# Kernel tuning notes

Hardware: AMD Instinct MI355X
Metric: run time of the kernel (lower is better)

Reference implementation:

```python
import jax, jax.numpy as jnp
import numpy as np

I_DIM, L_DIM, H_DIM, O_DIM = 1024, 1024, 2048, 512
HALT_H = max(4, H_DIM // 2)
BATCH = 4096


def setup_inputs() -> dict:
    key = jax.random.key(0)
    ks = jax.random.split(key, 14)
    s = 0.02
    gin = I_DIM + O_DIM
    jdim = L_DIM + O_DIM
    return {
        "inputs": jax.random.normal(ks[0], (BATCH, I_DIM), jnp.float32),
        "W_ih": jax.random.normal(ks[1], (3 * L_DIM, gin), jnp.float32) * s,
        "W_hh": jax.random.normal(ks[2], (3 * L_DIM, L_DIM), jnp.float32) * s,
        "b_ih": jax.random.normal(ks[3], (3 * L_DIM,), jnp.float32) * s,
        "b_hh": jax.random.normal(ks[4], (3 * L_DIM,), jnp.float32) * s,
        "aw1": jax.random.normal(ks[5], (H_DIM, jdim), jnp.float32) * s,
        "ab1": jax.random.normal(ks[6], (H_DIM,), jnp.float32) * s,
        "aw2": jax.random.normal(ks[7], (O_DIM, H_DIM), jnp.float32) * s,
        "ab2": jax.random.normal(ks[8], (O_DIM,), jnp.float32) * s,
        "hw1": jax.random.normal(ks[9], (HALT_H, jdim), jnp.float32) * s,
        "hb1": jax.random.normal(ks[10], (HALT_H,), jnp.float32) * s,
        "hw2": jax.random.normal(ks[11], (2, HALT_H), jnp.float32) * s,
        "hb2": jax.random.normal(ks[12], (2,), jnp.float32) * s,
        "inner_cycles": 4,
        "outer_steps": 8,
    }


def reference(inputs, W_ih, W_hh, b_ih, b_hh, aw1, ab1, aw2, ab2,
              hw1, hb1, hw2, hb2, inner_cycles, outer_steps):
    B = inputs.shape[0]
    L = W_hh.shape[1]
    O = aw2.shape[0]

    def gru_step(state, x_gates):
        # PyTorch GRUCell: gates ordered (r, z, n)
        h_gates = state @ W_hh.T + b_hh  # [B, 3L]
        xr, xz, xn = jnp.split(x_gates, 3, axis=-1)
        hr, hz, hn = jnp.split(h_gates, 3, axis=-1)
        r = jax.nn.sigmoid(xr + hr)
        z = jax.nn.sigmoid(xz + hz)
        n = jnp.tanh(xn + r * hn)
        return (1.0 - z) * n + z * state

    def outer(carry, _):
        state, ans = carry
        # gru_input is constant over inner cycles -> hoist input projection
        x = jnp.concatenate([inputs, ans], axis=-1)       # [B, I+O]
        x_gates = x @ W_ih.T + b_ih                        # [B, 3L]

        def inner(s, _):
            return gru_step(s, x_gates), None

        state, _ = jax.lax.scan(inner, state, None, length=inner_cycles)
        joint = jnp.concatenate([state, ans], axis=-1)     # [B, L+O]
        h1 = jax.nn.relu(joint @ aw1.T + ab1)
        logits = h1 @ aw2.T + ab2                          # [B, O]
        ans_new = jnp.tanh(logits)
        h2 = jax.nn.relu(joint @ hw1.T + hb1)
        halt = h2 @ hw2.T + hb2                            # [B, 2]
        return (state, ans_new), (logits, halt)

    state0 = jnp.zeros((B, L), inputs.dtype)
    ans0 = jnp.zeros((B, O), inputs.dtype)
    _, (answer_logits, halt_logits) = jax.lax.scan(
        outer, (state0, ans0), None, length=outer_steps)
    # stacked equivalents of the per-step lists: [outer_steps, B, O], [outer_steps, B, 2]
    return answer_logits, halt_logits
```

## Files before the change

### kernel.cpp

```cpp
#include <hip/hip_runtime.h>
#include <math.h>

#define BATCH 4096
#define LDIM 1024
#define HDIM 2048
#define ODIM 512
#define GDIM 3072
#define JDIM 1536
#define INNER 4
#define OUTER 8

using f16 = _Float16;
using f16x4 = __attribute__((ext_vector_type(4))) _Float16;
using f16x8 = __attribute__((ext_vector_type(8))) _Float16;
using f32x4 = __attribute__((ext_vector_type(4))) float;

typedef __attribute__((address_space(3))) void lds_void;
typedef __attribute__((address_space(1))) void glob_void;

__device__ __forceinline__ void gload16(const void* g, void* l) {
  __builtin_amdgcn_global_load_lds((const glob_void*)g, (lds_void*)l, 16, 0, 0);
}

#define MFMA16(a, b, c) __builtin_amdgcn_mfma_f32_16x16x32_f16(a, b, c, 0, 0, 0)
#define WAIT_VM(N) asm volatile("s_waitcnt vmcnt(" #N ")" ::: "memory")
#define SBAR asm volatile("s_barrier" ::: "memory")

__device__ __forceinline__ float fast_sigmoid(float x) {
  return __builtin_amdgcn_rcpf(1.0f + __expf(-x));
}
__device__ __forceinline__ float fast_tanh(float x) {
  return 1.0f - 2.0f * __builtin_amdgcn_rcpf(1.0f + __expf(2.0f * x));
}

__global__ __launch_bounds__(256) void convert_w(const float* __restrict__ src,
                                                 f16* __restrict__ dst, int n4) {
  int i = blockIdx.x * 256 + threadIdx.x;
  if (i >= n4) return;
  float4 v = ((const float4*)src)[i];
  f16x4 d = {(f16)v.x, (f16)v.y, (f16)v.z, (f16)v.w};
  *(f16x4*)&dst[(size_t)i * 4] = d;
}

__global__ __launch_bounds__(256) void convert_w2(const float* __restrict__ src,
                                                  f16* __restrict__ dst) {
  int idx = blockIdx.x * 256 + threadIdx.x;
  if (idx >= GDIM * 128) return;
  int row = idx >> 7, c4 = idx & 127;
  float4 v = *(const float4*)&src[(size_t)row * JDIM + 1024 + c4 * 4];
  f16x4 d = {(f16)v.x, (f16)v.y, (f16)v.z, (f16)v.w};
  *(f16x4*)&dst[(size_t)row * 512 + c4 * 4] = d;
}

template <int EPI>
__global__ __launch_bounds__(512, 1) void gemm_f16(
    const f16* __restrict__ A, const f16* __restrict__ W,
    const float* __restrict__ bias, const float* __restrict__ bias2,
    const f16* __restrict__ Xb,
    f16* __restrict__ Ch, f16* __restrict__ Cf, int N, int K, int lda, int ldw) {
  __shared__ f16 sA[2 * 2 * 128 * 32];
  __shared__ f16 sW[2 * 2 * 384 * 32];
  const int tid = threadIdx.x;
  const int w = tid >> 6, lane = tid & 63;
  const int wm = w >> 2, wn = w & 3;
  const int fr = lane & 15, quad = lane >> 4;
  const int nb = N / 384;
  const int m0 = (blockIdx.x / nb) * 128, n0 = (blockIdx.x % nb) * 384;

  const int swz_src = (((tid & 3) ^ ((tid >> 3) & 3)) * 8);
  const f16* pAst = A + (size_t)(m0 + (tid >> 2)) * lda + swz_src;
  const f16* pWst = W + (size_t)(n0 + (tid >> 2)) * ldw + swz_src;
  const size_t h128w = (size_t)128 * ldw;
  const int swr = ((quad ^ ((fr >> 1) & 3)) * 8);

  f32x4 acc[4][6] = {};
  const int NT = K >> 6;

#define STA(p, kh, kt)                                                \
  {                                                                   \
    int o = ((p) * 2 + (kh)) * 4096 + tid * 8;                        \
    gload16(pAst + (kt) * 64 + (kh) * 32, &sA[o]);                    \
  }
#define STW(p, kh, kt)                                                \
  {                                                                   \
    int o = ((p) * 2 + (kh)) * 12288 + tid * 8;                       \
    gload16(pWst + (kt) * 64 + (kh) * 32, &sW[o]);                    \
    gload16(pWst + h128w + (kt) * 64 + (kh) * 32, &sW[o + 4096]);     \
    gload16(pWst + 2 * h128w + (kt) * 64 + (kh) * 32, &sW[o + 8192]); \
  }
#define LDA(p, kk)                                                    \
  _Pragma("unroll") for (int i2 = 0; i2 < 4; ++i2) {                  \
    int rm = wm * 64 + i2 * 16 + fr;                                  \
    af[i2] = *(const f16x8*)&sA[((p) * 2 + (kk)) * 4096 + rm * 32 + swr]; \
  }
#define LDB(p, kk, nh)                                                \
  _Pragma("unroll") for (int j2 = 0; j2 < 3; ++j2) {                  \
    int rn = wn * 96 + ((nh) * 3 + j2) * 16 + fr;                     \
    bf[j2] = *(const f16x8*)&sW[((p) * 2 + (kk)) * 12288 + rn * 32 + swr]; \
  }
#define DOMFMA(nh)                                                    \
  __builtin_amdgcn_s_setprio(1);                                      \
  _Pragma("unroll") for (int i2 = 0; i2 < 4; ++i2)                    \
  _Pragma("unroll") for (int j2 = 0; j2 < 3; ++j2)                    \
      acc[i2][(nh) * 3 + j2] = MFMA16(af[i2], bf[j2], acc[i2][(nh) * 3 + j2]); \
  __builtin_amdgcn_s_setprio(0);

  STA(0, 0, 0); STW(0, 0, 0); STA(0, 1, 0); STW(0, 1, 0);

  for (int t = 0; t < NT; ++t) {
    const int p = t & 1, pn = p ^ 1;
    const bool pf = (t + 1 < NT);
    f16x8 af[4], bf[3];
    if (t == NT - 1) { WAIT_VM(0); } else { WAIT_VM(4); }
    SBAR;
    if (pf) STA(pn, 0, t + 1);
    LDA(p, 0); LDB(p, 0, 0);
    DOMFMA(0);
    SBAR;
    if (pf) STW(pn, 0, t + 1);
    LDB(p, 0, 1);
    DOMFMA(1);
    if (t == NT - 1) { WAIT_VM(0); } else { WAIT_VM(4); }
    SBAR;
    if (pf) STA(pn, 1, t + 1);
    LDA(p, 1); LDB(p, 1, 0);
    DOMFMA(0);
    SBAR;
    if (pf) STW(pn, 1, t + 1);
    LDB(p, 1, 1);
    DOMFMA(1);
  }
#undef STA
#undef STW
#undef LDA
#undef LDB
#undef DOMFMA

#pragma unroll
  for (int j = 0; j < 6; ++j) {
    int n = n0 + wn * 96 + j * 16 + fr;
    float bv;
    if (EPI == 3) bv = 0.0f;
    else if (EPI == 1) bv = (n < 2048) ? bias[n] : bias2[n - 2048];
    else bv = bias[n];
#pragma unroll
    for (int i = 0; i < 4; ++i) {
      int mb = m0 + wm * 64 + i * 16 + quad * 4;
      if (EPI == 0) {
        f16x4 o = {(f16)(acc[i][j][0] + bv), (f16)(acc[i][j][1] + bv),
                   (f16)(acc[i][j][2] + bv), (f16)(acc[i][j][3] + bv)};
        *(f16x4*)&Ch[((size_t)(mb >> 2) * N + n) * 4] = o;
      } else if (EPI == 3) {
        size_t off = ((size_t)(mb >> 2) * N + n) * 4;
        f16x4 b4 = *(const f16x4*)&Xb[off];
        f16x4 o = {(f16)(acc[i][j][0] + (float)b4[0]),
                   (f16)(acc[i][j][1] + (float)b4[1]),
                   (f16)(acc[i][j][2] + (float)b4[2]),
                   (f16)(acc[i][j][3] + (float)b4[3])};
        *(f16x4*)&Ch[off] = o;
      } else {
#pragma unroll
        for (int r = 0; r < 4; ++r) {
          int m = mb + r;
          float v = fmaxf(acc[i][j][r] + bv, 0.0f);
          if (n < 2048)
            Ch[(size_t)m * HDIM + n] = (f16)v;
          else
            Cf[(size_t)m * LDIM + (n - 2048)] = (f16)v;
        }
      }
    }
  }
}

__global__ __launch_bounds__(256, 2) void gemm_logits(
    const f16* __restrict__ A, const f16* __restrict__ W,
    const float* __restrict__ bias, float* __restrict__ Cout,
    f16* __restrict__ aJH, int N, int K) {
  __shared__ f16 sA[3][128 * 32];
  __shared__ f16 sW[3][64 * 32];
  const int tid = threadIdx.x;
  const int w = tid >> 6, lane = tid & 63;
  const int fr = lane & 15, quad = lane >> 4;
  const int m0 = blockIdx.y * 128, n0 = blockIdx.x * 64;
  const int swz_src = (((tid & 3) ^ ((tid >> 3) & 3)) * 8);
  const f16* pA = A + (size_t)(m0 + (tid >> 2)) * K + swz_src;
  const f16* pW = W + (size_t)(n0 + (tid >> 2)) * K + swz_src;
  const size_t rstep = (size_t)64 * K;
  const int swr = ((quad ^ ((fr >> 1) & 3)) * 8);

  f32x4 acc[2][4] = {};
  const int NT = K >> 5;

  auto stage = [&](int b, int k) {
    gload16(pA + k, &sA[b][tid * 8]);
    gload16(pA + rstep + k, &sA[b][tid * 8 + 2048]);
    gload16(pW + k, &sW[b][tid * 8]);
  };
  stage(0, 0);
  stage(1, 32);
  int bb = 0;
  for (int t = 0; t < NT; ++t) {
    if (t == NT - 1) { WAIT_VM(0); } else { WAIT_VM(3); }
    __builtin_amdgcn_s_barrier();
    if (t + 2 < NT) {
      int bn = bb + 2; if (bn >= 3) bn -= 3;
      stage(bn, (t + 2) * 32);
    }
    f16x8 af[2], bf[4];
#pragma unroll
    for (int i = 0; i < 2; ++i) {
      int rm = w * 32 + i * 16 + fr;
      af[i] = *(const f16x8*)&sA[bb][rm * 32 + swr];
    }
#pragma unroll
    for (int j = 0; j < 4; ++j) {
      int rn = j * 16 + fr;
      bf[j] = *(const f16x8*)&sW[bb][rn * 32 + swr];
    }
    __builtin_amdgcn_s_setprio(1);
#pragma unroll
    for (int i = 0; i < 2; ++i)
#pragma unroll
      for (int j = 0; j < 4; ++j) acc[i][j] = MFMA16(af[i], bf[j], acc[i][j]);
    __builtin_amdgcn_s_setprio(0);
    if (++bb == 3) bb = 0;
  }

#pragma unroll
  for (int j = 0; j < 4; ++j) {
    int n = n0 + j * 16 + fr;
    float bv = bias[n];
#pragma unroll
    for (int i = 0; i < 2; ++i) {
      int mb = m0 + w * 32 + i * 16 + quad * 4;
#pragma unroll
      for (int r = 0; r < 4; ++r) {
        int m = mb + r;
        float v = acc[i][j][r] + bv;
        Cout[(size_t)m * N + n] = v;
        aJH[(size_t)m * JDIM + 1024 + n] = (f16)fast_tanh(v);
      }
    }
  }
}

__global__ __launch_bounds__(256, 2) void gru_fused(
    const f16* __restrict__ inJ, const f16* __restrict__ Whh,
    const float* __restrict__ bhh, const f16* __restrict__ xgP,
    f16* __restrict__ outJ) {
  __shared__ f16 sA[3][128 * 32];
  __shared__ f16 sW0[3][64 * 32];
  __shared__ f16 sW1[3][64 * 32];
  __shared__ f16 sW2[3][64 * 32];
  const int tid = threadIdx.x;
  const int w = tid >> 6, lane = tid & 63;
  const int fr = lane & 15, quad = lane >> 4;
  const int flat = blockIdx.x;
  const int xcd = flat & 7, local = flat >> 3;
  const int n0 = (xcd * 2 + (local & 1)) * 64;
  const int m0 = (local >> 1) * 128;
  const int srow = w * 32 + (lane >> 2);
  const int scol = (((lane & 3) ^ ((lane >> 3) & 3)) * 8);
  const f16* pA = inJ + (size_t)(m0 + srow) * JDIM + scol;
  const size_t rstepA = (size_t)16 * JDIM;
  const int wrow = w * 16 + (lane >> 2);
  const f16* pW0 = Whh + (size_t)(n0 + wrow) * LDIM + scol;
  const f16* pW1 = pW0 + (size_t)LDIM * LDIM;
  const f16* pW2 = pW1 + (size_t)LDIM * LDIM;
  const int loA = w * 1024, loW = w * 512;

  f32x4 ar[2][4] = {}, az[2][4] = {}, an_[2][4] = {};
  const int NT = LDIM >> 5;

  auto stage = [&](int b, int k) {
    gload16(pA + k, &sA[b][loA]);
    gload16(pA + rstepA + k, &sA[b][loA + 512]);
    gload16(pW0 + k, &sW0[b][loW]);
    gload16(pW1 + k, &sW1[b][loW]);
    gload16(pW2 + k, &sW2[b][loW]);
  };
  stage(0, 0);
  stage(1, 32);
  int bb = 0;
  for (int t = 0; t < NT; ++t) {
    if (t == NT - 1) { WAIT_VM(0); } else { WAIT_VM(5); }
    __builtin_amdgcn_s_barrier();
    if (t + 2 < NT) {
      int bn = bb + 2; if (bn >= 3) bn -= 3;
      stage(bn, (t + 2) * 32);
    }
    f16x8 a_[2], w0[4], w1[4], w2[4];
#pragma unroll
    for (int i = 0; i < 2; ++i) {
      int rr = w * 32 + i * 16 + fr;
      a_[i] = *(const f16x8*)&sA[bb][rr * 32 + ((quad ^ ((rr >> 1) & 3)) << 3)];
    }
#pragma unroll
    for (int j = 0; j < 4; ++j) {
      int rw = j * 16 + fr;
      int wo = rw * 32 + ((quad ^ ((rw >> 1) & 3)) << 3);
      w0[j] = *(const f16x8*)&sW0[bb][wo];
      w1[j] = *(const f16x8*)&sW1[bb][wo];
      w2[j] = *(const f16x8*)&sW2[bb][wo];
    }
    __builtin_amdgcn_s_setprio(1);
#pragma unroll
    for (int i = 0; i < 2; ++i)
#pragma unroll
      for (int j = 0; j < 4; ++j) {
        ar[i][j] = MFMA16(a_[i], w0[j], ar[i][j]);
        az[i][j] = MFMA16(a_[i], w1[j], az[i][j]);
        an_[i][j] = MFMA16(a_[i], w2[j], an_[i][j]);
      }
    __builtin_amdgcn_s_setprio(0);
    if (++bb == 3) bb = 0;
  }

#pragma unroll
  for (int j = 0; j < 4; ++j) {
    int col = n0 + j * 16 + fr;
    float br = bhh[col], bz = bhh[col + LDIM], bn = bhh[col + 2 * LDIM];
#pragma unroll
    for (int i = 0; i < 2; ++i) {
      int mb = m0 + w * 32 + i * 16 + quad * 4;
      size_t xb = ((size_t)(mb >> 2) * GDIM + col) * 4;
      f16x4 x4r = *(const f16x4*)&xgP[xb];
      f16x4 x4z = *(const f16x4*)&xgP[xb + (size_t)LDIM * 4];
      f16x4 x4n = *(const f16x4*)&xgP[xb + (size_t)2 * LDIM * 4];
#pragma unroll
      for (int r = 0; r < 4; ++r) {
        int m = mb + r;
        size_t si = (size_t)m * JDIM + col;
        float sold = (float)inJ[si];
        float rg = fast_sigmoid((float)x4r[r] + ar[i][j][r] + br);
        float zg = fast_sigmoid((float)x4z[r] + az[i][j][r] + bz);
        float ng = fast_tanh((float)x4n[r] + rg * (an_[i][j][r] + bn));
        float o = (1.0f - zg) * ng + zg * sold;
        outJ[si] = (f16)o;
      }
    }
  }
}

__global__ __launch_bounds__(256) void halt_kernel(
    const f16* __restrict__ h2, const float* __restrict__ hw2,
    const float* __restrict__ hb2, float* __restrict__ out) {
  int wave = (blockIdx.x * 256 + threadIdx.x) >> 6;
  int lane = threadIdx.x & 63;
  if (wave >= BATCH) return;
  const f16* row = h2 + (size_t)wave * LDIM;
  float s0 = 0.0f, s1 = 0.0f;
#pragma unroll
  for (int k = lane; k < LDIM; k += 64) {
    float v = (float)row[k];
    s0 = fmaf(v, hw2[k], s0);
    s1 = fmaf(v, hw2[LDIM + k], s1);
  }
#pragma unroll
  for (int off = 32; off > 0; off >>= 1) {
    s0 += __shfl_xor(s0, off);
    s1 += __shfl_xor(s1, off);
  }
  if (lane == 0) {
    out[(size_t)wave * 2 + 0] = s0 + hb2[0];
    out[(size_t)wave * 2 + 1] = s1 + hb2[1];
  }
}

extern "C" void kernel_launch(void* const* d_in, const int* in_sizes, int n_in,
                              void* d_out, int out_size, void* d_ws, size_t ws_size,
                              hipStream_t stream) {
  const float* inputs = (const float*)d_in[0];
  const float* W_ih = (const float*)d_in[1];
  const float* W_hh = (const float*)d_in[2];
  const float* b_ih = (const float*)d_in[3];
  const float* b_hh = (const float*)d_in[4];
  const float* aw1 = (const float*)d_in[5];
  const float* ab1 = (const float*)d_in[6];
  const float* aw2 = (const float*)d_in[7];
  const float* ab2 = (const float*)d_in[8];
  const float* hw1 = (const float*)d_in[9];
  const float* hb1 = (const float*)d_in[10];
  const float* hw2 = (const float*)d_in[11];
  const float* hb2 = (const float*)d_in[12];

  float* out = (float*)d_out;
  float* logits_out = out;
  float* halt_out = out + (size_t)OUTER * BATCH * ODIM;

  char* p = (char*)d_ws;
  auto take = [&](size_t bytes) { char* q = p; p += (bytes + 255) & ~255ull; return q; };
  f16* xg = (f16*)take((size_t)BATCH * GDIM * 2);
  f16* inpF16 = xg;
  f16* WihF = xg + (size_t)BATCH * LDIM;
  f16* xgBase = (f16*)take((size_t)BATCH * GDIM * 2);
  f16* J0 = (f16*)take((size_t)BATCH * JDIM * 2);
  f16* J1 = (f16*)take((size_t)BATCH * JDIM * 2);
  f16* h2F = (f16*)take((size_t)BATCH * LDIM * 2);
  f16* WhhF = (f16*)take((size_t)GDIM * LDIM * 2);
  f16* WjF = (f16*)take((size_t)(HDIM + LDIM) * JDIM * 2);
  f16* aw2F = (f16*)take((size_t)ODIM * HDIM * 2);
  f16* W2F = (f16*)take((size_t)GDIM * 512 * 2);
  f16* h1 = xg;
  if ((size_t)(p - (char*)d_ws) > ws_size) return;

  (void)hipMemsetAsync(J0, 0, (size_t)BATCH * JDIM * 2, stream);

  auto conv = [&](const float* s, f16* d, size_t n) {
    int n4 = (int)(n / 4);
    convert_w<<<(n4 + 255) / 256, 256, 0, stream>>>(s, d, n4);
  };
  conv(inputs, inpF16, (size_t)BATCH * LDIM);
  conv(W_ih, WihF, (size_t)GDIM * JDIM);
  convert_w2<<<(GDIM * 128 + 255) / 256, 256, 0, stream>>>(W_ih, W2F);
  conv(W_hh, WhhF, (size_t)GDIM * LDIM);
  conv(aw1, WjF, (size_t)HDIM * JDIM);
  conv(hw1, WjF + (size_t)HDIM * JDIM, (size_t)LDIM * JDIM);
  conv(aw2, aw2F, (size_t)ODIM * HDIM);

  gemm_f16<0><<<(BATCH / 128) * (GDIM / 384), 512, 0, stream>>>(
      inpF16, WihF, b_ih, nullptr, nullptr, xgBase, nullptr,
      GDIM, LDIM, LDIM, JDIM);

  for (int s = 0; s < OUTER; ++s) {
    const f16* xgUse = xgBase;
    if (s > 0) {
      gemm_f16<3><<<(BATCH / 128) * (GDIM / 384), 512, 0, stream>>>(
          J0 + 1024, W2F, nullptr, nullptr, xgBase, xg, nullptr,
          GDIM, 512, JDIM, 512);
      xgUse = xg;
    }
    gru_fused<<<512, 256, 0, stream>>>(J0, WhhF, b_hh, xgUse, J1);
    gru_fused<<<512, 256, 0, stream>>>(J1, WhhF, b_hh, xgUse, J0);
    gru_fused<<<512, 256, 0, stream>>>(J0, WhhF, b_hh, xgUse, J1);
    gru_fused<<<512, 256, 0, stream>>>(J1, WhhF, b_hh, xgUse, J0);
    gemm_f16<1><<<(BATCH / 128) * ((HDIM + LDIM) / 384), 512, 0, stream>>>(
        J0, WjF, ab1, hb1, nullptr, h1, h2F, HDIM + LDIM, JDIM, JDIM, JDIM);
    gemm_logits<<<dim3(ODIM / 64, BATCH / 128), 256, 0, stream>>>(
        h1, aw2F, ab2, logits_out + (size_t)s * BATCH * ODIM, J0, ODIM, HDIM);
    halt_kernel<<<BATCH / 4, 256, 0, stream>>>(
        h2F, hw2, hb2, halt_out + (size_t)s * BATCH * 2);
  }
}
```

Baseline: 2.371 ms.

## Enlarge GRU and joint-MLP GEMM tiles for more operand reuse

The GRU kernel now uses 512-thread blocks, each computing a 128x128 tile per gate across 256 blocks instead of 128x64 tiles across 512 blocks. This changes the warp layout to 2x4 and drops the XCD-aware block mapping. A new 256x256-tile GEMM kernel replaces the 128x384 one for the joint MLP layer, with a per-block epilogue choosing between the h1 and h2 outputs. Both changes aim to cut global/LDS traffic per FLOP, at the cost of fewer blocks (lower occupancy, worse tail balance) and more registers per thread.

Result: slower. 2.523 ms (+6.4%).

```diff
diff --git a/kernel.cpp b/kernel.cpp
--- a/kernel.cpp
+++ b/kernel.cpp
@@ -53,11 +53,125 @@
 }
 
 template <int EPI>
-__global__ __launch_bounds__(512, 1) void gemm_f16(
+__global__ __launch_bounds__(512, 1) void gemm_256(
     const f16* __restrict__ A, const f16* __restrict__ W,
     const float* __restrict__ bias, const float* __restrict__ bias2,
     const f16* __restrict__ Xb,
     f16* __restrict__ Ch, f16* __restrict__ Cf, int N, int K, int lda, int ldw) {
+  __shared__ f16 sA[2 * 2 * 256 * 32];
+  __shared__ f16 sW[2 * 2 * 256 * 32];
+  const int tid = threadIdx.x;
+  const int w = tid >> 6, lane = tid & 63;
+  const int wm = w >> 2, wn = w & 3;
+  const int fr = lane & 15, quad = lane >> 4;
+  const int nb = N >> 8;
+  const int m0 = (blockIdx.x / nb) * 256, n0 = (blockIdx.x % nb) * 256;
+
+  const int swz_src = (((tid & 3) ^ ((tid >> 3) & 3)) * 8);
+  const f16* pAst = A + (size_t)(m0 + (tid >> 2)) * lda + swz_src;
+  const f16* pWst = W + (size_t)(n0 + (tid >> 2)) * ldw + swz_src;
+  const size_t h128a = (size_t)128 * lda;
+  const size_t h128w = (size_t)128 * ldw;
+  const int ldst = tid * 8;
+  const int swr = ((quad ^ ((fr >> 1) & 3)) * 8);
+
+  f32x4 acc[8][4] = {};
+  const int NT = K >> 6;
+
+#define STA(p, kh, kt)                                              \
+  {                                                                 \
+    int o = ((p) * 2 + (kh)) * 8192 + ldst;                         \
+    gload16(pAst + (kt) * 64 + (kh) * 32, &sA[o]);                  \
+    gload16(pAst + h128a + (kt) * 64 + (kh) * 32, &sA[o + 4096]);   \
+  }
+#define STW(p, kh, kt)                                              \
+  {                                                                 \
+    int o = ((p) * 2 + (kh)) * 8192 + ldst;                         \
+    gload16(pWst + (kt) * 64 + (kh) * 32, &sW[o]);                  \
+    gload16(pWst + h128w + (kt) * 64 + (kh) * 32, &sW[o + 4096]);   \
+  }
+#define LDB(p, kk)                                                  \
+  _Pragma("unroll") for (int j = 0; j < 4; ++j) {                   \
+    int rn = wn * 64 + j * 16 + fr;                                 \
+    bf[j] = *(const f16x8*)&sW[((p) * 2 + (kk)) * 8192 + rn * 32 + swr]; \
+  }
+#define LDA(p, kk, mh)                                              \
+  _Pragma("unroll") for (int i2 = 0; i2 < 4; ++i2) {                \
+    int rm = wm * 128 + (mh) * 64 + i2 * 16 + fr;                   \
+    af[i2] = *(const f16x8*)&sA[((p) * 2 + (kk)) * 8192 + rm * 32 + swr]; \
+  }
+#define DOMFMA(mh)                                                  \
+  __builtin_amdgcn_s_setprio(1);                                    \
+  _Pragma("unroll") for (int i2 = 0; i2 < 4; ++i2)                  \
+  _Pragma("unroll") for (int j = 0; j < 4; ++j)                     \
+      acc[(mh) * 4 + i2][j] = MFMA16(af[i2], bf[j], acc[(mh) * 4 + i2][j]); \
+  __builtin_amdgcn_s_setprio(0);
+
+  STA(0, 0, 0); STW(0, 0, 0); STA(0, 1, 0); STW(0, 1, 0);
+
+  for (int t = 0; t < NT; ++t) {
+    const int p = t & 1, pn = p ^ 1;
+    const bool pf = (t + 1 < NT);
+    f16x8 af[4], bf[4];
+    if (t == NT - 1) { WAIT_VM(0); } else { WAIT_VM(4); }
+    SBAR;
+    if (pf) STA(pn, 0, t + 1);
+    LDB(p, 0); LDA(p, 0, 0);
+    DOMFMA(0);
+    SBAR;
+    if (pf) STW(pn, 0, t + 1);
+    LDA(p, 0, 1);
+    DOMFMA(1);
+    if (t == NT - 1) { WAIT_VM(0); } else { WAIT_VM(4); }
+    SBAR;
+    if (pf) STA(pn, 1, t + 1);
+    LDB(p, 1); LDA(p, 1, 0);
+    DOMFMA(0);
+    SBAR;
+    if (pf) STW(pn, 1, t + 1);
+    LDA(p, 1, 1);
+    DOMFMA(1);
+  }
+#undef STA
+#undef STW
+#undef LDB
+#undef LDA
+#undef DOMFMA
+
+  bool is_h1 = true;
+  const float* bp = bias;
+  int nb0 = n0;
+  if (EPI == 1) {
+    is_h1 = (n0 < 2048);
+    bp = is_h1 ? bias : bias2;
+    nb0 = is_h1 ? n0 : n0 - 2048;
+  }
+#pragma unroll
+  for (int j = 0; j < 4; ++j) {
+    int n = nb0 + wn * 64 + j * 16 + fr;
+    float bv = bp[n];
+#pragma unroll
+    for (int i = 0; i < 8; ++i) {
+      int mb = m0 + wm * 128 + i * 16 + quad * 4;
+#pragma unroll
+      for (int r = 0; r < 4; ++r) {
+        int m = mb + r;
+        float v = fmaxf(acc[i][j][r] + bv, 0.0f);
+        if (is_h1)
+          Ch[(size_t)m * HDIM + n] = (f16)v;
+        else
+          Cf[(size_t)m * LDIM + n] = (f16)v;
+      }
+    }
+  }
+}
+
+template <int EPI>
+__global__ __launch_bounds__(512, 1) void gemm_384(
+    const f16* __restrict__ A, const f16* __restrict__ W,
+    const float* __restrict__ bias,
+    const f16* __restrict__ Xb,
+    f16* __restrict__ Ch, int N, int K, int lda, int ldw) {
   __shared__ f16 sA[2 * 2 * 128 * 32];
   __shared__ f16 sW[2 * 2 * 384 * 32];
   const int tid = threadIdx.x;
@@ -139,10 +253,7 @@
 #pragma unroll
   for (int j = 0; j < 6; ++j) {
     int n = n0 + wn * 96 + j * 16 + fr;
-    float bv;
-    if (EPI == 3) bv = 0.0f;
-    else if (EPI == 1) bv = (n < 2048) ? bias[n] : bias2[n - 2048];
-    else bv = bias[n];
+    float bv = (EPI == 3) ? 0.0f : bias[n];
 #pragma unroll
     for (int i = 0; i < 4; ++i) {
       int mb = m0 + wm * 64 + i * 16 + quad * 4;
@@ -150,7 +261,7 @@
         f16x4 o = {(f16)(acc[i][j][0] + bv), (f16)(acc[i][j][1] + bv),
                    (f16)(acc[i][j][2] + bv), (f16)(acc[i][j][3] + bv)};
         *(f16x4*)&Ch[((size_t)(mb >> 2) * N + n) * 4] = o;
-      } else if (EPI == 3) {
+      } else {
         size_t off = ((size_t)(mb >> 2) * N + n) * 4;
         f16x4 b4 = *(const f16x4*)&Xb[off];
         f16x4 o = {(f16)(acc[i][j][0] + (float)b4[0]),
@@ -158,16 +269,6 @@
                    (f16)(acc[i][j][2] + (float)b4[2]),
                    (f16)(acc[i][j][3] + (float)b4[3])};
         *(f16x4*)&Ch[off] = o;
-      } else {
-#pragma unroll
-        for (int r = 0; r < 4; ++r) {
-          int m = mb + r;
-          float v = fmaxf(acc[i][j][r] + bv, 0.0f);
-          if (n < 2048)
-            Ch[(size_t)m * HDIM + n] = (f16)v;
-          else
-            Cf[(size_t)m * LDIM + (n - 2048)] = (f16)v;
-        }
       }
     }
   }
@@ -245,60 +346,55 @@
   }
 }
 
-__global__ __launch_bounds__(256, 2) void gru_fused(
+__global__ __launch_bounds__(512, 1) void gru_fused(
     const f16* __restrict__ inJ, const f16* __restrict__ Whh,
     const float* __restrict__ bhh, const f16* __restrict__ xgP,
     f16* __restrict__ outJ) {
   __shared__ f16 sA[3][128 * 32];
-  __shared__ f16 sW0[3][64 * 32];
-  __shared__ f16 sW1[3][64 * 32];
-  __shared__ f16 sW2[3][64 * 32];
+  __shared__ f16 sW0[3][128 * 32];
+  __shared__ f16 sW1[3][128 * 32];
+  __shared__ f16 sW2[3][128 * 32];
   const int tid = threadIdx.x;
   const int w = tid >> 6, lane = tid & 63;
   const int fr = lane & 15, quad = lane >> 4;
-  const int flat = blockIdx.x;
-  const int xcd = flat & 7, local = flat >> 3;
-  const int n0 = (xcd * 2 + (local & 1)) * 64;
-  const int m0 = (local >> 1) * 128;
-  const int srow = w * 32 + (lane >> 2);
-  const int scol = (((lane & 3) ^ ((lane >> 3) & 3)) * 8);
-  const f16* pA = inJ + (size_t)(m0 + srow) * JDIM + scol;
-  const size_t rstepA = (size_t)16 * JDIM;
-  const int wrow = w * 16 + (lane >> 2);
-  const f16* pW0 = Whh + (size_t)(n0 + wrow) * LDIM + scol;
+  const int wm = w >> 2, wn = w & 3;
+  const int n0 = (blockIdx.x & 7) * 128;
+  const int m0 = (blockIdx.x >> 3) * 128;
+  const int swz_src = (((tid & 3) ^ ((tid >> 3) & 3)) * 8);
+  const f16* pA = inJ + (size_t)(m0 + (tid >> 2)) * JDIM + swz_src;
+  const f16* pW0 = Whh + (size_t)(n0 + (tid >> 2)) * LDIM + swz_src;
   const f16* pW1 = pW0 + (size_t)LDIM * LDIM;
   const f16* pW2 = pW1 + (size_t)LDIM * LDIM;
-  const int loA = w * 1024, loW = w * 512;
-
-  f32x4 ar[2][4] = {}, az[2][4] = {}, an_[2][4] = {};
+  const int swr = ((quad ^ ((fr >> 1) & 3)) * 8);
+
+  f32x4 ar[4][2] = {}, az[4][2] = {}, an_[4][2] = {};
   const int NT = LDIM >> 5;
 
   auto stage = [&](int b, int k) {
-    gload16(pA + k, &sA[b][loA]);
-    gload16(pA + rstepA + k, &sA[b][loA + 512]);
-    gload16(pW0 + k, &sW0[b][loW]);
-    gload16(pW1 + k, &sW1[b][loW]);
-    gload16(pW2 + k, &sW2[b][loW]);
+    gload16(pA + k, &sA[b][tid * 8]);
+    gload16(pW0 + k, &sW0[b][tid * 8]);
+    gload16(pW1 + k, &sW1[b][tid * 8]);
+    gload16(pW2 + k, &sW2[b][tid * 8]);
   };
   stage(0, 0);
   stage(1, 32);
   int bb = 0;
   for (int t = 0; t < NT; ++t) {
-    if (t == NT - 1) { WAIT_VM(0); } else { WAIT_VM(5); }
+    if (t == NT - 1) { WAIT_VM(0); } else { WAIT_VM(4); }
     __builtin_amdgcn_s_barrier();
     if (t + 2 < NT) {
       int bn = bb + 2; if (bn >= 3) bn -= 3;
       stage(bn, (t + 2) * 32);
     }
-    f16x8 a_[2], w0[4], w1[4], w2[4];
-#pragma unroll
-    for (int i = 0; i < 2; ++i) {
-      int rr = w * 32 + i * 16 + fr;
+    f16x8 a_[4], w0[2], w1[2], w2[2];
+#pragma unroll
+    for (int i = 0; i < 4; ++i) {
+      int rr = wm * 64 + i * 16 + fr;
       a_[i] = *(const f16x8*)&sA[bb][rr * 32 + ((quad ^ ((rr >> 1) & 3)) << 3)];
     }
 #pragma unroll
-    for (int j = 0; j < 4; ++j) {
-      int rw = j * 16 + fr;
+    for (int j = 0; j < 2; ++j) {
+      int rw = wn * 32 + j * 16 + fr;
       int wo = rw * 32 + ((quad ^ ((rw >> 1) & 3)) << 3);
       w0[j] = *(const f16x8*)&sW0[bb][wo];
       w1[j] = *(const f16x8*)&sW1[bb][wo];
@@ -306,9 +402,9 @@
     }
     __builtin_amdgcn_s_setprio(1);
 #pragma unroll
-    for (int i = 0; i < 2; ++i)
-#pragma unroll
-      for (int j = 0; j < 4; ++j) {
+    for (int i = 0; i < 4; ++i)
+#pragma unroll
+      for (int j = 0; j < 2; ++j) {
         ar[i][j] = MFMA16(a_[i], w0[j], ar[i][j]);
         az[i][j] = MFMA16(a_[i], w1[j], az[i][j]);
         an_[i][j] = MFMA16(a_[i], w2[j], an_[i][j]);
@@ -318,12 +414,12 @@
   }
 
 #pragma unroll
-  for (int j = 0; j < 4; ++j) {
-    int col = n0 + j * 16 + fr;
+  for (int j = 0; j < 2; ++j) {
+    int col = n0 + wn * 32 + j * 16 + fr;
     float br = bhh[col], bz = bhh[col + LDIM], bn = bhh[col + 2 * LDIM];
 #pragma unroll
-    for (int i = 0; i < 2; ++i) {
-      int mb = m0 + w * 32 + i * 16 + quad * 4;
+    for (int i = 0; i < 4; ++i) {
+      int mb = m0 + wm * 64 + i * 16 + quad * 4;
       size_t xb = ((size_t)(mb >> 2) * GDIM + col) * 4;
       f16x4 x4r = *(const f16x4*)&xgP[xb];
       f16x4 x4z = *(const f16x4*)&xgP[xb + (size_t)LDIM * 4];
@@ -419,23 +515,21 @@
   conv(hw1, WjF + (size_t)HDIM * JDIM, (size_t)LDIM * JDIM);
   conv(aw2, aw2F, (size_t)ODIM * HDIM);
 
-  gemm_f16<0><<<(BATCH / 128) * (GDIM / 384), 512, 0, stream>>>(
-      inpF16, WihF, b_ih, nullptr, nullptr, xgBase, nullptr,
-      GDIM, LDIM, LDIM, JDIM);
+  gemm_384<0><<<(BATCH / 128) * (GDIM / 384), 512, 0, stream>>>(
+      inpF16, WihF, b_ih, nullptr, xgBase, GDIM, LDIM, LDIM, JDIM);
 
   for (int s = 0; s < OUTER; ++s) {
     const f16* xgUse = xgBase;
     if (s > 0) {
-      gemm_f16<3><<<(BATCH / 128) * (GDIM / 384), 512, 0, stream>>>(
-          J0 + 1024, W2F, nullptr, nullptr, xgBase, xg, nullptr,
-          GDIM, 512, JDIM, 512);
+      gemm_384<3><<<(BATCH / 128) * (GDIM / 384), 512, 0, stream>>>(
+          J0 + 1024, W2F, nullptr, xgBase, xg, GDIM, 512, JDIM, 512);
       xgUse = xg;
     }
-    gru_fused<<<512, 256, 0, stream>>>(J0, WhhF, b_hh, xgUse, J1);
-    gru_fused<<<512, 256, 0, stream>>>(J1, WhhF, b_hh, xgUse, J0);
-    gru_fused<<<512, 256, 0, stream>>>(J0, WhhF, b_hh, xgUse, J1);
-    gru_fused<<<512, 256, 0, stream>>>(J1, WhhF, b_hh, xgUse, J0);
-    gemm_f16<1><<<(BATCH / 128) * ((HDIM + LDIM) / 384), 512, 0, stream>>>(
+    gru_fused<<<256, 512, 0, stream>>>(J0, WhhF, b_hh, xgUse, J1);
+    gru_fused<<<256, 512, 0, stream>>>(J1, WhhF, b_hh, xgUse, J0);
+    gru_fused<<<256, 512, 0, stream>>>(J0, WhhF, b_hh, xgUse, J1);
+    gru_fused<<<256, 512, 0, stream>>>(J1, WhhF, b_hh, xgUse, J0);
+    gemm_256<1><<<(BATCH / 256) * ((HDIM + LDIM) / 256), 512, 0, stream>>>(
         J0, WjF, ab1, hb1, nullptr, h1, h2F, HDIM + LDIM, JDIM, JDIM, JDIM);
     gemm_logits<<<dim3(ODIM / 64, BATCH / 128), 256, 0, stream>>>(
         h1, aw2F, ab2, logits_out + (size_t)s * BATCH * ODIM, J0, ODIM, HDIM);
```
